# Kernel tuning notes

Hardware: AMD Instinct MI355X
Metric: run time of the kernel (lower is better)

Reference implementation:

```python
import jax, jax.numpy as jnp
import numpy as np

VOCAB, D, PAD, SPARSITY = 6, 32, 5, 0.15


def setup_inputs() -> dict:
    key = jax.random.key(0)
    ks = jax.random.split(key, 16)
    x = jax.random.randint(ks[0], (256, 4096), 0, VOCAB, dtype=jnp.int32)
    s = 0.1
    emb = jax.random.normal(ks[1], (VOCAB, D), jnp.float32) * s
    return {
        "x": x,
        "emb": emb,
        # selector: D -> D//2 -> 1 (sigmoid)
        "sel_w1": jax.random.normal(ks[2], (D, D // 2), jnp.float32) * s,
        "sel_b1": jnp.zeros((D // 2,), jnp.float32),
        "sel_w2": jax.random.normal(ks[3], (D // 2, 1), jnp.float32) * s,
        "sel_b2": jnp.zeros((1,), jnp.float32),
        # approximator: D -> D -> D
        "app_w1": jax.random.normal(ks[4], (D, D), jnp.float32) * s,
        "app_b1": jnp.zeros((D,), jnp.float32),
        "app_w2": jax.random.normal(ks[5], (D, D), jnp.float32) * s,
        "app_b2": jnp.zeros((D,), jnp.float32),
        # classifier: D -> D//2 -> 1 (sigmoid)
        "cls_w1": jax.random.normal(ks[6], (D, D // 2), jnp.float32) * s,
        "cls_b1": jnp.zeros((D // 2,), jnp.float32),
        "cls_w2": jax.random.normal(ks[7], (D // 2, 1), jnp.float32) * s,
        "cls_b2": jnp.zeros((1,), jnp.float32),
    }


def reference(x, emb, sel_w1, sel_b1, sel_w2, sel_b2,
              app_w1, app_b1, app_w2, app_b2,
              cls_w1, cls_b1, cls_w2, cls_b2):
    B, S = x.shape
    k = max(1, int(S * SPARSITY))
    table = emb.at[PAD].set(0.0)            # padding_idx row is zero
    e = table[x]                            # [B, S, D]
    # selector scores (tiny MLP + sigmoid)
    h = jax.nn.relu(e @ sel_w1 + sel_b1)
    scores = jax.nn.sigmoid((h @ sel_w2 + sel_b2).squeeze(-1))  # [B, S]
    _, top_idx = jax.lax.top_k(scores, k)   # [B, k]
    sel = jnp.take_along_axis(e, top_idx[..., None], axis=1)    # [B, k, D]
    a = jax.nn.relu(sel @ app_w1 + app_b1) @ app_w2 + app_b2    # [B, k, D]
    pooled = a.mean(axis=1)                 # [B, D]
    c = jax.nn.relu(pooled @ cls_w1 + cls_b1)
    pred = jax.nn.sigmoid((c @ cls_w2 + cls_b2).squeeze(-1))    # [B]
    return pred, top_idx, scores
```

## Files before the change

kernel.cpp:

```cpp
#include <hip/hip_runtime.h>
#include <math.h>

#define VOCABN 6
#define DIM 32
#define PADI 5
#define BATCH 256
#define SEQ 4096
#define KSEL 614

__device__ __forceinline__ float lut6(float s0, float s1, float s2, float s3,
                                      float s4, float s5, int tk) {
    float r = s0;
    r = (tk == 1) ? s1 : r;
    r = (tk == 2) ? s2 : r;
    r = (tk == 3) ? s3 : r;
    r = (tk == 4) ? s4 : r;
    r = (tk == 5) ? s5 : r;
    return r;
}

__global__ __launch_bounds__(1024) void fused_row_kernel(
    const int* __restrict__ x,
    const float* __restrict__ emb,
    const float* __restrict__ sel_w1, const float* __restrict__ sel_b1,
    const float* __restrict__ sel_w2, const float* __restrict__ sel_b2,
    const float* __restrict__ app_w1, const float* __restrict__ app_b1,
    const float* __restrict__ app_w2, const float* __restrict__ app_b2,
    const float* __restrict__ cls_w1, const float* __restrict__ cls_b1,
    const float* __restrict__ cls_w2, const float* __restrict__ cls_b2,
    float* __restrict__ out_pred,
    float* __restrict__ out_topidx,
    float* __restrict__ out_scores) {
    const int b = blockIdx.x;
    const int t = threadIdx.x;
    const int lane = t & 63;
    const int w = t >> 6;

    __shared__ float s_emb[VOCABN * DIM];
    __shared__ float s_appw1[DIM * DIM];
    __shared__ float s_appw2[DIM * DIM];
    __shared__ float s_appb1[DIM], s_appb2[DIM];
    __shared__ float s_clsw1[DIM * (DIM / 2)];
    __shared__ float s_clsb1[DIM / 2], s_clsw2[DIM / 2];
    __shared__ float s_clsb2v;
    __shared__ float s_ah[VOCABN * DIM];
    __shared__ float s_a[VOCABN * DIM];
    __shared__ int s_wtot[16][VOCABN];
    __shared__ int s_sel[VOCABN], s_base[VOCABN];
    __shared__ float s_pooled[DIM], s_c[DIM / 2];

    const int4 tw = *(const int4*)(x + (size_t)b * SEQ + t * 4);

    s_appw1[t] = app_w1[t];
    s_appw2[t] = app_w2[t];
    if (t < 512) s_clsw1[t] = cls_w1[t];
    else if (t < 704) { int i = t - 512; s_emb[i] = (i >= PADI * DIM) ? 0.f : emb[i]; }
    else if (t < 736) { int i = t - 704; s_appb1[i] = app_b1[i]; }
    else if (t < 768) { int i = t - 736; s_appb2[i] = app_b2[i]; }
    else if (t < 784) { int i = t - 768; s_clsb1[i] = cls_b1[i]; }
    else if (t < 800) { int i = t - 784; s_clsw2[i] = cls_w2[i]; }
    else if (t == 800) s_clsb2v = cls_b2[0];

    int sv = lane >> 3; if (sv >= VOCABN) sv -= VOCABN;
    const int j0 = (lane & 7) * 2;
    const float2 bj = *(const float2*)(sel_b1 + j0);
    const float2 wj = *(const float2*)(sel_w2 + j0);
    float h0 = bj.x, h1 = bj.y;
    if (sv != PADI) {
        const float4* e4 = (const float4*)(emb + sv * DIM);
        #pragma unroll
        for (int q = 0; q < 8; ++q) {
            const float4 e = e4[q];
            const float2 wa = *(const float2*)(sel_w1 + (q * 4 + 0) * (DIM / 2) + j0);
            const float2 wb = *(const float2*)(sel_w1 + (q * 4 + 1) * (DIM / 2) + j0);
            const float2 wc = *(const float2*)(sel_w1 + (q * 4 + 2) * (DIM / 2) + j0);
            const float2 wd = *(const float2*)(sel_w1 + (q * 4 + 3) * (DIM / 2) + j0);
            h0 += e.x * wa.x + e.y * wb.x + e.z * wc.x + e.w * wd.x;
            h1 += e.x * wa.y + e.y * wb.y + e.z * wc.y + e.w * wd.y;
        }
    }
    float part = fmaxf(h0, 0.f) * wj.x + fmaxf(h1, 0.f) * wj.y;
    part += __shfl_xor(part, 1, 64);
    part += __shfl_xor(part, 2, 64);
    part += __shfl_xor(part, 4, 64);
    const float sig = 1.f / (1.f + expf(-(part + sel_b2[0])));
    const float sc0 = __shfl(sig,  0, 64);
    const float sc1 = __shfl(sig,  8, 64);
    const float sc2 = __shfl(sig, 16, 64);
    const float sc3 = __shfl(sig, 24, 64);
    const float sc4 = __shfl(sig, 32, 64);
    const float sc5 = __shfl(sig, 40, 64);

    int tok[4];
    tok[0] = tw.x; tok[1] = tw.y; tok[2] = tw.z; tok[3] = tw.w;

    {
        float4 f;
        f.x = lut6(sc0, sc1, sc2, sc3, sc4, sc5, tok[0]);
        f.y = lut6(sc0, sc1, sc2, sc3, sc4, sc5, tok[1]);
        f.z = lut6(sc0, sc1, sc2, sc3, sc4, sc5, tok[2]);
        f.w = lut6(sc0, sc1, sc2, sc3, sc4, sc5, tok[3]);
        *(float4*)(out_scores + (size_t)b * SEQ + t * 4) = f;
    }

    int cnt[VOCABN], val[VOCABN];
    #pragma unroll
    for (int v = 0; v < VOCABN; ++v) {
        int c = 0;
        #pragma unroll
        for (int i = 0; i < 4; ++i) c += (tok[i] == v) ? 1 : 0;
        cnt[v] = c; val[v] = c;
    }
    for (int off = 1; off < 64; off <<= 1) {
        #pragma unroll
        for (int v = 0; v < VOCABN; ++v) {
            int up = __shfl_up(val[v], off, 64);
            if (lane >= off) val[v] += up;
        }
    }
    if (lane == 63) {
        #pragma unroll
        for (int v = 0; v < VOCABN; ++v) s_wtot[w][v] = val[v];
    }
    __syncthreads();

    int excl[VOCABN];
    #pragma unroll
    for (int v = 0; v < VOCABN; ++v) {
        int pre = 0;
        for (int ww = 0; ww < w; ++ww) pre += s_wtot[ww][v];
        excl[v] = pre + val[v] - cnt[v];
    }

    if (t == 0) {
        float scv[VOCABN] = {sc0, sc1, sc2, sc3, sc4, sc5};
        int rank[VOCABN];
        #pragma unroll
        for (int v = 0; v < VOCABN; ++v) {
            int r = 0;
            for (int u = 0; u < VOCABN; ++u) {
                if (scv[u] > scv[v]) ++r;
                else if (scv[u] == scv[v] && u < v) ++r;
            }
            rank[r] = v;
        }
        int rem = KSEL;
        for (int r = 0; r < VOCABN; ++r) {
            const int v = rank[r];
            int tot = 0;
            for (int ww = 0; ww < 16; ++ww) tot += s_wtot[ww][v];
            const int take = tot < rem ? tot : rem;
            s_base[v] = KSEL - rem;
            s_sel[v] = take;
            rem -= take;
        }
    }
    if (t >= 128 && t < 128 + VOCABN * DIM) {
        const int i = t - 128, v = i >> 5, j = i & 31;
        float acc = s_appb1[j];
        #pragma unroll
        for (int d = 0; d < DIM; ++d) acc += s_emb[v * DIM + d] * s_appw1[d * DIM + j];
        s_ah[i] = fmaxf(acc, 0.f);
    }
    __syncthreads();

    #pragma unroll
    for (int v = 0; v < VOCABN; ++v) {
        int p = excl[v];
        const int sel = s_sel[v];
        const int bs = s_base[v];
        #pragma unroll
        for (int i = 0; i < 4; ++i) {
            if (tok[i] == v) {
                if (p < sel) out_topidx[(size_t)b * KSEL + bs + p] = (float)(t * 4 + i);
                ++p;
            }
        }
    }

    if (t >= 128 && t < 128 + VOCABN * DIM) {
        const int i = t - 128, v = i >> 5, d = i & 31;
        float acc = s_appb2[d];
        #pragma unroll
        for (int j = 0; j < DIM; ++j) acc += s_ah[v * DIM + j] * s_appw2[j * DIM + d];
        s_a[i] = acc;
    }
    __syncthreads();

    if (t < DIM) {
        float acc = 0.f;
        #pragma unroll
        for (int v = 0; v < VOCABN; ++v) acc += (float)s_sel[v] * s_a[v * DIM + t];
        s_pooled[t] = acc / (float)KSEL;
    }
    __syncthreads();
    if (t < DIM / 2) {
        float acc = s_clsb1[t];
        #pragma unroll
        for (int d = 0; d < DIM; ++d) acc += s_pooled[d] * s_clsw1[d * (DIM / 2) + t];
        s_c[t] = fmaxf(acc, 0.f);
    }
    __syncthreads();
    if (t == 0) {
        float z = s_clsb2v;
        #pragma unroll
        for (int j = 0; j < DIM / 2; ++j) z += s_c[j] * s_clsw2[j];
        out_pred[b] = 1.f / (1.f + expf(-z));
    }
}

extern "C" void kernel_launch(void* const* d_in, const int* in_sizes, int n_in,
                              void* d_out, int out_size, void* d_ws, size_t ws_size,
                              hipStream_t stream) {
    const int*   x      = (const int*)  d_in[0];
    const float* emb    = (const float*)d_in[1];
    const float* sel_w1 = (const float*)d_in[2];
    const float* sel_b1 = (const float*)d_in[3];
    const float* sel_w2 = (const float*)d_in[4];
    const float* sel_b2 = (const float*)d_in[5];
    const float* app_w1 = (const float*)d_in[6];
    const float* app_b1 = (const float*)d_in[7];
    const float* app_w2 = (const float*)d_in[8];
    const float* app_b2 = (const float*)d_in[9];
    const float* cls_w1 = (const float*)d_in[10];
    const float* cls_b1 = (const float*)d_in[11];
    const float* cls_w2 = (const float*)d_in[12];
    const float* cls_b2 = (const float*)d_in[13];

    float* out = (float*)d_out;
    float* out_pred   = out;
    float* out_topidx = out + BATCH;
    float* out_scores = out + BATCH + BATCH * KSEL;

    fused_row_kernel<<<BATCH, 1024, 0, stream>>>(
        x, emb, sel_w1, sel_b1, sel_w2, sel_b2,
        app_w1, app_b1, app_w2, app_b2,
        cls_w1, cls_b1, cls_w2, cls_b2,
        out_pred, out_topidx, out_scores);
}
```

Baseline: 102.0 us.

## Cut block barriers by computing selection redundantly and finishing the MLP chain in one wavefront

The kernel now stages the selector weights in shared memory and moves the token-count scan ahead of a single barrier. Every thread then computes the per-vocab ranks, totals and selection counts redundantly instead of thread 0 publishing them through shared memory. The approximator, pooling and classifier chain runs inside one wavefront using shuffles, which removes four further __syncthreads. The cost is extra redundant ALU work per thread and a serial dependency chain inside one wave, in exchange for fewer block-wide synchronisations and fewer global loads of small weights.

```diff
diff --git a/kernel.cpp b/kernel.cpp
--- a/kernel.cpp
+++ b/kernel.cpp
@@ -37,62 +37,77 @@
     const int w = t >> 6;
 
     __shared__ float s_emb[VOCABN * DIM];
+    __shared__ float s_selw1[DIM * (DIM / 2)];
+    __shared__ float s_selb1[DIM / 2], s_selw2[DIM / 2];
+    __shared__ float s_selb2, s_clsb2v;
     __shared__ float s_appw1[DIM * DIM];
     __shared__ float s_appw2[DIM * DIM];
     __shared__ float s_appb1[DIM], s_appb2[DIM];
     __shared__ float s_clsw1[DIM * (DIM / 2)];
     __shared__ float s_clsb1[DIM / 2], s_clsw2[DIM / 2];
-    __shared__ float s_clsb2v;
-    __shared__ float s_ah[VOCABN * DIM];
-    __shared__ float s_a[VOCABN * DIM];
     __shared__ int s_wtot[16][VOCABN];
-    __shared__ int s_sel[VOCABN], s_base[VOCABN];
-    __shared__ float s_pooled[DIM], s_c[DIM / 2];
 
     const int4 tw = *(const int4*)(x + (size_t)b * SEQ + t * 4);
 
     s_appw1[t] = app_w1[t];
     s_appw2[t] = app_w2[t];
-    if (t < 512) s_clsw1[t] = cls_w1[t];
-    else if (t < 704) { int i = t - 512; s_emb[i] = (i >= PADI * DIM) ? 0.f : emb[i]; }
-    else if (t < 736) { int i = t - 704; s_appb1[i] = app_b1[i]; }
-    else if (t < 768) { int i = t - 736; s_appb2[i] = app_b2[i]; }
-    else if (t < 784) { int i = t - 768; s_clsb1[i] = cls_b1[i]; }
-    else if (t < 800) { int i = t - 784; s_clsw2[i] = cls_w2[i]; }
-    else if (t == 800) s_clsb2v = cls_b2[0];
+    if (t < 512) s_selw1[t] = sel_w1[t];
+    else s_clsw1[t - 512] = cls_w1[t - 512];
+    if (t < 192) s_emb[t] = (t >= PADI * DIM) ? 0.f : emb[t];
+    else if (t < 208) { int i = t - 192; s_selb1[i] = sel_b1[i]; }
+    else if (t < 224) { int i = t - 208; s_selw2[i] = sel_w2[i]; }
+    else if (t < 256) { int i = t - 224; s_appb1[i] = app_b1[i]; }
+    else if (t < 288) { int i = t - 256; s_appb2[i] = app_b2[i]; }
+    else if (t < 304) { int i = t - 288; s_clsb1[i] = cls_b1[i]; }
+    else if (t < 320) { int i = t - 304; s_clsw2[i] = cls_w2[i]; }
+    else if (t == 320) s_selb2 = sel_b2[0];
+    else if (t == 321) s_clsb2v = cls_b2[0];
+
+    int tok[4];
+    tok[0] = tw.x; tok[1] = tw.y; tok[2] = tw.z; tok[3] = tw.w;
+
+    int cnt[VOCABN], val[VOCABN];
+    #pragma unroll
+    for (int v = 0; v < VOCABN; ++v) {
+        int c = 0;
+        #pragma unroll
+        for (int i = 0; i < 4; ++i) c += (tok[i] == v) ? 1 : 0;
+        cnt[v] = c; val[v] = c;
+    }
+    for (int off = 1; off < 64; off <<= 1) {
+        #pragma unroll
+        for (int v = 0; v < VOCABN; ++v) {
+            int up = __shfl_up(val[v], off, 64);
+            if (lane >= off) val[v] += up;
+        }
+    }
+    if (lane == 63) {
+        #pragma unroll
+        for (int v = 0; v < VOCABN; ++v) s_wtot[w][v] = val[v];
+    }
+
+    __syncthreads();
 
     int sv = lane >> 3; if (sv >= VOCABN) sv -= VOCABN;
     const int j0 = (lane & 7) * 2;
-    const float2 bj = *(const float2*)(sel_b1 + j0);
-    const float2 wj = *(const float2*)(sel_w2 + j0);
-    float h0 = bj.x, h1 = bj.y;
-    if (sv != PADI) {
-        const float4* e4 = (const float4*)(emb + sv * DIM);
-        #pragma unroll
-        for (int q = 0; q < 8; ++q) {
-            const float4 e = e4[q];
-            const float2 wa = *(const float2*)(sel_w1 + (q * 4 + 0) * (DIM / 2) + j0);
-            const float2 wb = *(const float2*)(sel_w1 + (q * 4 + 1) * (DIM / 2) + j0);
-            const float2 wc = *(const float2*)(sel_w1 + (q * 4 + 2) * (DIM / 2) + j0);
-            const float2 wd = *(const float2*)(sel_w1 + (q * 4 + 3) * (DIM / 2) + j0);
-            h0 += e.x * wa.x + e.y * wb.x + e.z * wc.x + e.w * wd.x;
-            h1 += e.x * wa.y + e.y * wb.y + e.z * wc.y + e.w * wd.y;
-        }
-    }
-    float part = fmaxf(h0, 0.f) * wj.x + fmaxf(h1, 0.f) * wj.y;
+    float h0 = s_selb1[j0], h1 = s_selb1[j0 + 1];
+    #pragma unroll
+    for (int d = 0; d < DIM; ++d) {
+        const float e = s_emb[sv * DIM + d];
+        h0 += e * s_selw1[d * (DIM / 2) + j0];
+        h1 += e * s_selw1[d * (DIM / 2) + j0 + 1];
+    }
+    float part = fmaxf(h0, 0.f) * s_selw2[j0] + fmaxf(h1, 0.f) * s_selw2[j0 + 1];
     part += __shfl_xor(part, 1, 64);
     part += __shfl_xor(part, 2, 64);
     part += __shfl_xor(part, 4, 64);
-    const float sig = 1.f / (1.f + expf(-(part + sel_b2[0])));
+    const float sig = 1.f / (1.f + expf(-(part + s_selb2)));
     const float sc0 = __shfl(sig,  0, 64);
     const float sc1 = __shfl(sig,  8, 64);
     const float sc2 = __shfl(sig, 16, 64);
     const float sc3 = __shfl(sig, 24, 64);
     const float sc4 = __shfl(sig, 32, 64);
     const float sc5 = __shfl(sig, 40, 64);
-
-    int tok[4];
-    tok[0] = tw.x; tok[1] = tw.y; tok[2] = tw.z; tok[3] = tw.w;
 
     {
         float4 f;
@@ -103,26 +118,37 @@
         *(float4*)(out_scores + (size_t)b * SEQ + t * 4) = f;
     }
 
-    int cnt[VOCABN], val[VOCABN];
-    #pragma unroll
-    for (int v = 0; v < VOCABN; ++v) {
-        int c = 0;
-        #pragma unroll
-        for (int i = 0; i < 4; ++i) c += (tok[i] == v) ? 1 : 0;
-        cnt[v] = c; val[v] = c;
-    }
-    for (int off = 1; off < 64; off <<= 1) {
-        #pragma unroll
-        for (int v = 0; v < VOCABN; ++v) {
-            int up = __shfl_up(val[v], off, 64);
-            if (lane >= off) val[v] += up;
-        }
-    }
-    if (lane == 63) {
-        #pragma unroll
-        for (int v = 0; v < VOCABN; ++v) s_wtot[w][v] = val[v];
-    }
-    __syncthreads();
+    const float scv[VOCABN] = {sc0, sc1, sc2, sc3, sc4, sc5};
+    int totv[VOCABN];
+    #pragma unroll
+    for (int v = 0; v < VOCABN; ++v) {
+        int tot = 0;
+        for (int ww = 0; ww < 16; ++ww) tot += s_wtot[ww][v];
+        totv[v] = tot;
+    }
+    int rk[VOCABN];
+    #pragma unroll
+    for (int v = 0; v < VOCABN; ++v) {
+        int r = 0;
+        #pragma unroll
+        for (int u = 0; u < VOCABN; ++u) {
+            if (scv[u] > scv[v]) ++r;
+            else if (scv[u] == scv[v] && u < v) ++r;
+        }
+        rk[v] = r;
+    }
+    int selv[VOCABN], basev[VOCABN];
+    #pragma unroll
+    for (int v = 0; v < VOCABN; ++v) {
+        int before = 0;
+        #pragma unroll
+        for (int u = 0; u < VOCABN; ++u) before += (rk[u] < rk[v]) ? totv[u] : 0;
+        const int base = before < KSEL ? before : KSEL;
+        int take = KSEL - base;
+        take = totv[v] < take ? totv[v] : take;
+        basev[v] = base;
+        selv[v] = take > 0 ? take : 0;
+    }
 
     int excl[VOCABN];
     #pragma unroll
@@ -131,81 +157,50 @@
         for (int ww = 0; ww < w; ++ww) pre += s_wtot[ww][v];
         excl[v] = pre + val[v] - cnt[v];
     }
-
-    if (t == 0) {
-        float scv[VOCABN] = {sc0, sc1, sc2, sc3, sc4, sc5};
-        int rank[VOCABN];
-        #pragma unroll
-        for (int v = 0; v < VOCABN; ++v) {
-            int r = 0;
-            for (int u = 0; u < VOCABN; ++u) {
-                if (scv[u] > scv[v]) ++r;
-                else if (scv[u] == scv[v] && u < v) ++r;
-            }
-            rank[r] = v;
-        }
-        int rem = KSEL;
-        for (int r = 0; r < VOCABN; ++r) {
-            const int v = rank[r];
-            int tot = 0;
-            for (int ww = 0; ww < 16; ++ww) tot += s_wtot[ww][v];
-            const int take = tot < rem ? tot : rem;
-            s_base[v] = KSEL - rem;
-            s_sel[v] = take;
-            rem -= take;
-        }
-    }
-    if (t >= 128 && t < 128 + VOCABN * DIM) {
-        const int i = t - 128, v = i >> 5, j = i & 31;
-        float acc = s_appb1[j];
-        #pragma unroll
-        for (int d = 0; d < DIM; ++d) acc += s_emb[v * DIM + d] * s_appw1[d * DIM + j];
-        s_ah[i] = fmaxf(acc, 0.f);
-    }
-    __syncthreads();
-
     #pragma unroll
     for (int v = 0; v < VOCABN; ++v) {
         int p = excl[v];
-        const int sel = s_sel[v];
-        const int bs = s_base[v];
         #pragma unroll
         for (int i = 0; i < 4; ++i) {
             if (tok[i] == v) {
-                if (p < sel) out_topidx[(size_t)b * KSEL + bs + p] = (float)(t * 4 + i);
+                if (p < selv[v]) out_topidx[(size_t)b * KSEL + basev[v] + p] = (float)(t * 4 + i);
                 ++p;
             }
         }
     }
 
-    if (t >= 128 && t < 128 + VOCABN * DIM) {
-        const int i = t - 128, v = i >> 5, d = i & 31;
-        float acc = s_appb2[d];
-        #pragma unroll
-        for (int j = 0; j < DIM; ++j) acc += s_ah[v * DIM + j] * s_appw2[j * DIM + d];
-        s_a[i] = acc;
-    }
-    __syncthreads();
-
-    if (t < DIM) {
-        float acc = 0.f;
-        #pragma unroll
-        for (int v = 0; v < VOCABN; ++v) acc += (float)s_sel[v] * s_a[v * DIM + t];
-        s_pooled[t] = acc / (float)KSEL;
-    }
-    __syncthreads();
-    if (t < DIM / 2) {
-        float acc = s_clsb1[t];
-        #pragma unroll
-        for (int d = 0; d < DIM; ++d) acc += s_pooled[d] * s_clsw1[d * (DIM / 2) + t];
-        s_c[t] = fmaxf(acc, 0.f);
-    }
-    __syncthreads();
-    if (t == 0) {
-        float z = s_clsb2v;
-        #pragma unroll
-        for (int j = 0; j < DIM / 2; ++j) z += s_c[j] * s_clsw2[j];
-        out_pred[b] = 1.f / (1.f + expf(-z));
+    if (w == 1) {
+        float pooled = 0.f;
+        #pragma unroll
+        for (int v = 0; v < VOCABN; ++v) {
+            float ah = 0.f;
+            if (lane < DIM) {
+                ah = s_appb1[lane];
+                #pragma unroll
+                for (int d = 0; d < DIM; ++d) ah += s_emb[v * DIM + d] * s_appw1[d * DIM + lane];
+                ah = fmaxf(ah, 0.f);
+            }
+            float av = (lane < DIM) ? s_appb2[lane] : 0.f;
+            #pragma unroll
+            for (int j = 0; j < DIM; ++j) {
+                const float ahj = __shfl(ah, j, 64);
+                if (lane < DIM) av += ahj * s_appw2[j * DIM + lane];
+            }
+            pooled += (float)selv[v] * av;
+        }
+        pooled *= (1.f / (float)KSEL);
+        float c = (lane < DIM / 2) ? s_clsb1[lane] : 0.f;
+        #pragma unroll
+        for (int d = 0; d < DIM; ++d) {
+            const float pd = __shfl(pooled, d, 64);
+            if (lane < DIM / 2) c += pd * s_clsw1[d * (DIM / 2) + lane];
+        }
+        float term = (lane < DIM / 2) ? fmaxf(c, 0.f) * s_clsw2[lane] : 0.f;
+        term += __shfl_xor(term, 1, 64);
+        term += __shfl_xor(term, 2, 64);
+        term += __shfl_xor(term, 4, 64);
+        term += __shfl_xor(term, 8, 64);
+        if (lane == 0) out_pred[b] = 1.f / (1.f + expf(-(term + s_clsb2v)));
     }
 }
 
```

Measured after the change: 99.42 us. 1.03x faster.
